# Optimization experiments

Measured on AMD Instinct MI355X. Metric: run time of the kernel, lower is better.

The kernel has to match this reference:

```python
import jax, jax.numpy as jnp
import numpy as np

NUM_HEADS = 32
MICRO_BATCHES = 2
TOP_K = 2
LN_EPS = 1e-5


def _mha(x, scale, bias, wq, wk, wv, wo):
    # Pre-LN multi-head self-attention with residual (RealSelfAttention).
    B, S, D = x.shape
    H = NUM_HEADS
    hd = D // H
    res = x
    mu = jnp.mean(x, axis=-1, keepdims=True)
    xc = x - mu
    var = jnp.mean(xc * xc, axis=-1, keepdims=True)
    xn = xc / jnp.sqrt(var + LN_EPS) * scale + bias
    q = (xn @ wq.T).reshape(B, S, H, hd).transpose(0, 2, 1, 3)
    k = (xn @ wk.T).reshape(B, S, H, hd).transpose(0, 2, 1, 3)
    v = (xn @ wv.T).reshape(B, S, H, hd).transpose(0, 2, 1, 3)
    scores = jnp.einsum('bhqd,bhkd->bhqk', q, k) * (1.0 / np.sqrt(hd).astype(np.float32))
    attn = jax.nn.softmax(scores, axis=-1)
    o = jnp.einsum('bhqk,bhkd->bhqd', attn, v).transpose(0, 2, 1, 3).reshape(B, S, D)
    return o @ wo.T + res


def setup_inputs() -> dict:
    key = jax.random.key(0)
    D, E, F = 1024, 8, 4096
    B, S = 4, 1024
    ks = jax.random.split(key, 16)
    w = lambda k, shape: (jax.random.normal(k, shape, dtype=jnp.float32) * 0.02)
    return {
        'x': jax.random.normal(ks[0], (B, S, D), dtype=jnp.float32),
        'ln1_scale': jnp.ones((D,), jnp.float32),
        'ln1_bias': jnp.zeros((D,), jnp.float32),
        'wq1': w(ks[1], (D, D)), 'wk1': w(ks[2], (D, D)),
        'wv1': w(ks[3], (D, D)), 'wo1': w(ks[4], (D, D)),
        'gate_w': w(ks[5], (E, D)),
        'exp_w1': w(ks[6], (E, F, D)), 'exp_b1': jnp.zeros((E, F), jnp.float32),
        'exp_w2': w(ks[7], (E, D, F)), 'exp_b2': jnp.zeros((E, D), jnp.float32),
        'ln2_scale': jnp.ones((D,), jnp.float32),
        'ln2_bias': jnp.zeros((D,), jnp.float32),
        'wq2': w(ks[8], (D, D)), 'wk2': w(ks[9], (D, D)),
        'wv2': w(ks[10], (D, D)), 'wo2': w(ks[11], (D, D)),
    }


def reference(x, ln1_scale, ln1_bias, wq1, wk1, wv1, wo1, gate_w,
              exp_w1, exp_b1, exp_w2, exp_b2,
              ln2_scale, ln2_bias, wq2, wk2, wv2, wo2):
    B, S, D = x.shape
    E = exp_w1.shape[0]
    # PreOps: attention layer L (per-sample, so full-batch apply == per-microbatch apply)
    y = _mha(x, ln1_scale, ln1_bias, wq1, wk1, wv1, wo1)
    # Gate: logits + top-k indices computed in source but never applied to tokens.
    flat = y.reshape(B * S, D)
    logits = flat @ gate_w.T
    _ = jax.lax.top_k(logits, TOP_K)  # indices unused downstream (faithful to source)
    # Dispatch (all_to_all on 1 device == identity): per-microbatch flat tokens are
    # chunked equally across local experts.
    T = (B // MICRO_BATCHES) * S            # tokens per microbatch
    toks = y.reshape(MICRO_BATCHES, E, T // E, D)
    h = jax.nn.gelu(jnp.einsum('metd,efd->metf', toks, exp_w1) + exp_b1[None, :, None, :],
                    approximate=False)
    eo = jnp.einsum('metf,edf->metd', h, exp_w2) + exp_b2[None, :, None, :]
    # Combine (identity) + PostOps: attention layer L+1
    z = eo.reshape(B, S, D)
    out = _mha(z, ln2_scale, ln2_bias, wq2, wk2, wv2, wo2)
    return out
```

## Files before the change

### kernel.cpp

```cpp
#include <hip/hip_runtime.h>

typedef __attribute__((ext_vector_type(8))) short bf16x8;
typedef __attribute__((ext_vector_type(4))) float f32x4;
typedef __attribute__((ext_vector_type(4))) short short4v;

#define DEV __device__ __forceinline__

DEV short f2bf(float f) {
  union { float f; unsigned u; } x; x.f = f;
  unsigned r = x.u + 0x7fffu + ((x.u >> 16) & 1u);
  return (short)(r >> 16);
}

#define GL2LDS16(g, l) __builtin_amdgcn_global_load_lds(                      \
    (const __attribute__((address_space(1))) void*)(g),                       \
    (__attribute__((address_space(3))) void*)(l), 16, 0, 0)

__global__ __launch_bounds__(256) void k_cast_bf16(const float* __restrict__ s,
                                                   short* __restrict__ d, int n4) {
  int i = blockIdx.x * 256 + threadIdx.x;
  if (i >= n4) return;
  float4 v = ((const float4*)s)[i];
  short4v o;
  o[0] = f2bf(v.x); o[1] = f2bf(v.y); o[2] = f2bf(v.z); o[3] = f2bf(v.w);
  ((short4v*)d)[i] = o;
}

__global__ __launch_bounds__(256)
void k_ln(const float* __restrict__ X, const float* __restrict__ G,
          const float* __restrict__ Bi, short* __restrict__ Y) {
  const int row = blockIdx.x, t = threadIdx.x;
  const float4 v = ((const float4*)(X + (size_t)row * 1024))[t];
  float s = v.x + v.y + v.z + v.w;
  float s2 = v.x * v.x + v.y * v.y + v.z * v.z + v.w * v.w;
#pragma unroll
  for (int m = 1; m < 64; m <<= 1) { s += __shfl_xor(s, m); s2 += __shfl_xor(s2, m); }
  __shared__ float rs[4], rq[4];
  const int w = t >> 6, lane = t & 63;
  if (lane == 0) { rs[w] = s; rq[w] = s2; }
  __syncthreads();
  s = rs[0] + rs[1] + rs[2] + rs[3];
  s2 = rq[0] + rq[1] + rq[2] + rq[3];
  const float mu = s * (1.f / 1024.f);
  const float var = s2 * (1.f / 1024.f) - mu * mu;
  const float rstd = rsqrtf(var + 1e-5f);
  const float4 g = ((const float4*)G)[t];
  const float4 bi = ((const float4*)Bi)[t];
  short4v o;
  o[0] = f2bf((v.x - mu) * rstd * g.x + bi.x);
  o[1] = f2bf((v.y - mu) * rstd * g.y + bi.y);
  o[2] = f2bf((v.z - mu) * rstd * g.z + bi.z);
  o[3] = f2bf((v.w - mu) * rstd * g.w + bi.w);
  ((short4v*)(Y + (size_t)row * 1024))[t] = o;
}

template <int EPI, int EXPERT, int BN>
__global__ __launch_bounds__(256)
void k_gemm_bt(const short* __restrict__ A, const short* __restrict__ Bt,
               void* __restrict__ Cv, const float* __restrict__ Res,
               const float* __restrict__ Bias, int M, int N, int K) {
  constexpr int NF = BN / 32;
  constexpr int BR = BN / 64;
  __shared__ __attribute__((aligned(16))) short As[2][128 * 32];
  __shared__ __attribute__((aligned(16))) short Bs[2][BN * 32];
  const int tid = threadIdx.x;
  const int w = tid >> 6, lane = tid & 63;
  const int r16 = lane & 15, kg = lane >> 4;
  const int wr = w >> 1, wc = w & 1;

  size_t rowBase = (size_t)blockIdx.y * 128;
  size_t bOff = 0, biasOff = 0;
  if constexpr (EXPERT) {
    int e = blockIdx.z >> 1, mb = blockIdx.z & 1;
    rowBase += (size_t)(mb * 8 + e) * 256;
    bOff = (size_t)e * N * K;
    biasOff = (size_t)e * N;
  }
  const size_t col0 = (size_t)blockIdx.x * BN;
  const short* Ab = A + rowBase * K;
  const short* Bb = Bt + bOff + col0 * K;

  f32x4 acc[4][NF] = {};

  auto stage = [&](int buf, int k0) {
#pragma unroll
    for (int i = 0; i < 2; ++i) {
      int c = (i * 4 + w) * 64 + lane;
      int row = c >> 2;
      int sl = (c & 3) ^ (row & 3);
      GL2LDS16(Ab + (size_t)row * K + k0 + sl * 8, (char*)As[buf] + (size_t)(i * 4 + w) * 1024);
    }
#pragma unroll
    for (int i = 0; i < BR; ++i) {
      int c = (i * 4 + w) * 64 + lane;
      int row = c >> 2;
      int sl = (c & 3) ^ (row & 3);
      GL2LDS16(Bb + (size_t)row * K + k0 + sl * 8, (char*)Bs[buf] + (size_t)(i * 4 + w) * 1024);
    }
  };

  stage(0, 0);
  __syncthreads();
  int cur = 0;
  for (int k0 = 0; k0 < K; k0 += 32) {
    if (k0 + 32 < K) stage(cur ^ 1, k0 + 32);
    bf16x8 af[4], bg[NF];
#pragma unroll
    for (int m = 0; m < 4; ++m) {
      int row = wr * 64 + m * 16 + r16;
      af[m] = *(const bf16x8*)(As[cur] + row * 32 + (kg ^ (row & 3)) * 8);
    }
#pragma unroll
    for (int n = 0; n < NF; ++n) {
      int row = wc * (BN / 2) + n * 16 + r16;
      bg[n] = *(const bf16x8*)(Bs[cur] + row * 32 + (kg ^ (row & 3)) * 8);
    }
#pragma unroll
    for (int m = 0; m < 4; ++m)
#pragma unroll
      for (int n = 0; n < NF; ++n)
        acc[m][n] = __builtin_amdgcn_mfma_f32_16x16x32_bf16(af[m], bg[n], acc[m][n], 0, 0, 0);
    __syncthreads();
    cur ^= 1;
  }

#pragma unroll
  for (int m = 0; m < 4; ++m) {
    size_t grow0 = rowBase + wr * 64 + m * 16 + kg * 4;
#pragma unroll
    for (int n = 0; n < NF; ++n) {
      size_t gcol = col0 + wc * (BN / 2) + n * 16 + r16;
#pragma unroll
      for (int r = 0; r < 4; ++r) {
        size_t idx = (grow0 + r) * (size_t)N + gcol;
        float v = acc[m][n][r];
        if constexpr (EPI == 1 || EPI == 4) v += Res[idx];
        if constexpr (EPI == 2 || EPI == 3) v += Bias[biasOff + gcol];
        if constexpr (EPI == 2) v = 0.5f * v * (1.f + erff(v * 0.70710678118654752f));
        if constexpr (EPI <= 2) ((short*)Cv)[idx] = f2bf(v);
        else                    ((float*)Cv)[idx] = v;
      }
    }
  }
}

__global__ __launch_bounds__(256, 3)
void k_attn(const short* __restrict__ QKV, short* __restrict__ O) {
  const int qt = blockIdx.x, h = blockIdx.y, b = blockIdx.z;
  const int tid = threadIdx.x, w = tid >> 6, lane = tid & 63;
  const int r16 = lane & 15, kg = lane >> 4;

  __shared__ __attribute__((aligned(16))) short Kl[2][128 * 32];
  __shared__ __attribute__((aligned(16))) short Vt[2][32 * 128];
  __shared__ __attribute__((aligned(16))) short Pl[4][16 * 128];

  const size_t tb = (size_t)b * 1024;
  const int qbase = qt * 128 + w * 32;

  bf16x8 aq[2];
#pragma unroll
  for (int f = 0; f < 2; ++f)
    aq[f] = *(const bf16x8*)(QKV + (tb + qbase + f * 16 + r16) * 3072 + h * 32 + kg * 8);

  f32x4 acc[2][2] = {};
  float lreg[2][4] = {};
  const float scale = 0.17677669529663687f;

  auto stageK = [&](int bid, int kc) {
#pragma unroll
    for (int i = 0; i < 2; ++i) {
      int c = (i * 4 + w) * 64 + lane;
      int row = c >> 2;
      int sl = (c & 3) ^ (row & 3);
      GL2LDS16(QKV + (tb + kc * 128 + row) * 3072 + 1024 + h * 32 + sl * 8,
               (char*)Kl[bid] + (size_t)(i * 4 + w) * 1024);
    }
  };

  stageK(0, 0);
  {
    int c0 = tid,        vr0 = c0 >> 2, d00 = (c0 & 3) * 8;
    int c1 = 256 + tid,  vr1 = c1 >> 2, d01 = (c1 & 3) * 8;
    bf16x8 v0 = *(const bf16x8*)(QKV + (tb + vr0) * 3072 + 2048 + h * 32 + d00);
    bf16x8 v1 = *(const bf16x8*)(QKV + (tb + vr1) * 3072 + 2048 + h * 32 + d01);
#pragma unroll
    for (int j = 0; j < 8; ++j) {
      int da = d00 + j, db = d01 + j;
      Vt[0][((da * 128 + vr0) ^ ((da & 7) << 3))] = v0[j];
      Vt[0][((db * 128 + vr1) ^ ((db & 7) << 3))] = v1[j];
    }
  }
  __syncthreads();

  int bi = 0;
  for (int kc = 0; kc < 8; ++kc) {
    bf16x8 nv0, nv1;
    int nvr0 = 0, nd0 = 0, nvr1 = 0, nd1 = 0;
    if (kc < 7) {
      stageK(bi ^ 1, kc + 1);
      const short* Vg = QKV + (tb + (size_t)(kc + 1) * 128) * 3072 + 2048 + h * 32;
      int c0 = tid;       nvr0 = c0 >> 2; nd0 = (c0 & 3) * 8;
      int c1 = 256 + tid; nvr1 = c1 >> 2; nd1 = (c1 & 3) * 8;
      nv0 = *(const bf16x8*)(Vg + (size_t)nvr0 * 3072 + nd0);
      nv1 = *(const bf16x8*)(Vg + (size_t)nvr1 * 3072 + nd1);
    }

    f32x4 s[2][8];
#pragma unroll
    for (int kt = 0; kt < 8; ++kt) {
      int row = kt * 16 + r16;
      bf16x8 bk = *(const bf16x8*)(Kl[bi] + row * 32 + (kg ^ (row & 3)) * 8);
      f32x4 zz = {0.f, 0.f, 0.f, 0.f};
      s[0][kt] = __builtin_amdgcn_mfma_f32_16x16x32_bf16(aq[0], bk, zz, 0, 0, 0);
      s[1][kt] = __builtin_amdgcn_mfma_f32_16x16x32_bf16(aq[1], bk, zz, 0, 0, 0);
    }

#pragma unroll
    for (int f = 0; f < 2; ++f)
#pragma unroll
      for (int r = 0; r < 4; ++r) {
        float sum = 0.f;
#pragma unroll
        for (int kt = 0; kt < 8; ++kt) {
          float p = __expf(s[f][kt][r] * scale);
          s[f][kt][r] = p;
          sum += p;
        }
#pragma unroll
        for (int m = 1; m < 16; m <<= 1) sum += __shfl_xor(sum, m);
        lreg[f][r] += sum;
      }

    short* P = Pl[w];
#pragma unroll
    for (int f = 0; f < 2; ++f) {
#pragma unroll
      for (int kt = 0; kt < 8; ++kt)
#pragma unroll
        for (int r = 0; r < 4; ++r) {
          int row = kg * 4 + r;
          P[((row * 128 + kt * 16 + r16) ^ ((row & 7) << 3))] = f2bf(s[f][kt][r]);
        }
#pragma unroll
      for (int ks = 0; ks < 4; ++ks) {
        bf16x8 pa = *(const bf16x8*)(P + ((r16 * 128 + ks * 32 + kg * 8) ^ ((r16 & 7) << 3)));
#pragma unroll
        for (int dt = 0; dt < 2; ++dt) {
          int vrow = dt * 16 + r16;
          bf16x8 bv = *(const bf16x8*)(Vt[bi] + ((vrow * 128 + ks * 32 + kg * 8) ^ ((vrow & 7) << 3)));
          acc[f][dt] = __builtin_amdgcn_mfma_f32_16x16x32_bf16(pa, bv, acc[f][dt], 0, 0, 0);
        }
      }
    }

    if (kc < 7) {
#pragma unroll
      for (int j = 0; j < 8; ++j) {
        int da = nd0 + j, db = nd1 + j;
        Vt[bi ^ 1][((da * 128 + nvr0) ^ ((da & 7) << 3))] = nv0[j];
        Vt[bi ^ 1][((db * 128 + nvr1) ^ ((db & 7) << 3))] = nv1[j];
      }
    }

    __syncthreads();
    bi ^= 1;
  }

#pragma unroll
  for (int f = 0; f < 2; ++f)
#pragma unroll
    for (int r = 0; r < 4; ++r) {
      float inv = 1.f / lreg[f][r];
      size_t qrow = tb + qbase + f * 16 + kg * 4 + r;
#pragma unroll
      for (int dt = 0; dt < 2; ++dt)
        O[qrow * 1024 + h * 32 + dt * 16 + r16] = f2bf(acc[f][dt][r] * inv);
    }
}

extern "C" void kernel_launch(void* const* d_in, const int* in_sizes, int n_in,
                              void* d_out, int out_size, void* d_ws, size_t ws_size,
                              hipStream_t stream) {
  const float* x    = (const float*)d_in[0];
  const float* ln1s = (const float*)d_in[1];
  const float* ln1b = (const float*)d_in[2];
  const float* wq1  = (const float*)d_in[3];
  const float* wk1  = (const float*)d_in[4];
  const float* wv1  = (const float*)d_in[5];
  const float* wo1  = (const float*)d_in[6];
  const float* ew1  = (const float*)d_in[8];
  const float* eb1  = (const float*)d_in[9];
  const float* ew2  = (const float*)d_in[10];
  const float* eb2  = (const float*)d_in[11];
  const float* ln2s = (const float*)d_in[12];
  const float* ln2b = (const float*)d_in[13];
  const float* wq2  = (const float*)d_in[14];
  const float* wk2  = (const float*)d_in[15];
  const float* wv2  = (const float*)d_in[16];
  const float* wo2  = (const float*)d_in[17];

  char* ws = (char*)d_ws;
  size_t off = 0;
  auto alloc = [&](size_t bytes) {
    char* p = ws + off;
    off += (bytes + 255) & ~(size_t)255;
    return p;
  };
  short* wqkv1b = (short*)alloc(3072ull * 1024 * 2);
  short* wo1b   = (short*)alloc(1024ull * 1024 * 2);
  short* wqkv2b = (short*)alloc(3072ull * 1024 * 2);
  short* wo2b   = (short*)alloc(1024ull * 1024 * 2);
  short* ew1b   = (short*)alloc(8ull * 4096 * 1024 * 2);
  short* ew2b   = (short*)alloc(8ull * 1024 * 4096 * 2);
  short* xnb    = (short*)alloc(4096ull * 1024 * 2);
  short* qkvo   = (short*)alloc(4096ull * 4096 * 2);
  short* ybf    = (short*)alloc(4096ull * 1024 * 2);
  float* zf     = (float*)alloc(4096ull * 1024 * 4);
  (void)ws_size; (void)in_sizes; (void)n_in; (void)out_size;

  short* QKV = qkvo;
  short* Ob  = qkvo + 4096ull * 3072;
  short* hb  = qkvo;

  auto cast = [&](const float* s, short* d, size_t n) {
    int n4 = (int)(n / 4);
    k_cast_bf16<<<(n4 + 255) / 256, 256, 0, stream>>>(s, d, n4);
  };
  cast(wq1, wqkv1b,           1048576);
  cast(wk1, wqkv1b + 1048576, 1048576);
  cast(wv1, wqkv1b + 2097152, 1048576);
  cast(wo1, wo1b,             1048576);
  cast(wq2, wqkv2b,           1048576);
  cast(wk2, wqkv2b + 1048576, 1048576);
  cast(wv2, wqkv2b + 2097152, 1048576);
  cast(wo2, wo2b,             1048576);
  cast(ew1, ew1b, 8ull * 4096 * 1024);
  cast(ew2, ew2b, 8ull * 1024 * 4096);

  k_ln<<<4096, 256, 0, stream>>>(x, ln1s, ln1b, xnb);
  k_gemm_bt<0, 0, 128><<<dim3(24, 32, 1), 256, 0, stream>>>(xnb, wqkv1b, QKV, nullptr, nullptr, 4096, 3072, 1024);
  k_attn<<<dim3(8, 32, 4), 256, 0, stream>>>(QKV, Ob);
  k_gemm_bt<1, 0, 64><<<dim3(16, 32, 1), 256, 0, stream>>>(Ob, wo1b, ybf, x, nullptr, 4096, 1024, 1024);
  k_gemm_bt<2, 1, 128><<<dim3(32, 2, 16), 256, 0, stream>>>(ybf, ew1b, hb, nullptr, eb1, 256, 4096, 1024);
  k_gemm_bt<3, 1, 64><<<dim3(16, 2, 16), 256, 0, stream>>>(hb, ew2b, zf, nullptr, eb2, 256, 1024, 4096);
  k_ln<<<4096, 256, 0, stream>>>(zf, ln2s, ln2b, xnb);
  k_gemm_bt<0, 0, 128><<<dim3(24, 32, 1), 256, 0, stream>>>(xnb, wqkv2b, QKV, nullptr, nullptr, 4096, 3072, 1024);
  k_attn<<<dim3(8, 32, 4), 256, 0, stream>>>(QKV, Ob);
  k_gemm_bt<4, 0, 64><<<dim3(16, 32, 1), 256, 0, stream>>>(Ob, wo2b, (float*)d_out, zf, nullptr, 4096, 1024, 1024);
}
```

Before: 574.8 us.

## Fuse fp32 expert-weight conversion into GEMM loads and remap block indices

Removes the separate cast kernels for the two large expert weight tensors (64M floats). The expert GEMMs now read fp32 weights directly into registers, convert them to bf16 and write them to LDS after the MFMA step, so the load overlaps compute. All grids become 1D with a remapped block order, which groups blocks sharing weight tiles (expert-interleaved, and row tiles grouped by 8 for the dense GEMMs) to improve L2 reuse. The expert GEMMs now read twice the weight bytes per tile through register-staged loads instead of async global-to-LDS, which raises register pressure.

Result: faster. 543.1 us (-5.5%).

```diff
diff --git a/kernel.cpp b/kernel.cpp
--- a/kernel.cpp
+++ b/kernel.cpp
@@ -54,11 +54,11 @@
   ((short4v*)(Y + (size_t)row * 1024))[t] = o;
 }
 
-template <int EPI, int EXPERT, int BN>
+template <int EPI, int EXPERT, int BN, int BF32>
 __global__ __launch_bounds__(256)
-void k_gemm_bt(const short* __restrict__ A, const short* __restrict__ Bt,
+void k_gemm_bt(const short* __restrict__ A, const void* __restrict__ Btv,
                void* __restrict__ Cv, const float* __restrict__ Res,
-               const float* __restrict__ Bias, int M, int N, int K) {
+               const float* __restrict__ Bias, int M, int N, int K, int xt) {
   constexpr int NF = BN / 32;
   constexpr int BR = BN / 64;
   __shared__ __attribute__((aligned(16))) short As[2][128 * 32];
@@ -68,21 +68,29 @@
   const int r16 = lane & 15, kg = lane >> 4;
   const int wr = w >> 1, wc = w & 1;
 
-  size_t rowBase = (size_t)blockIdx.y * 128;
-  size_t bOff = 0, biasOff = 0;
+  const int bid = blockIdx.x;
+  int bx;
+  size_t rowBase, bOff = 0, biasOff = 0;
   if constexpr (EXPERT) {
-    int e = blockIdx.z >> 1, mb = blockIdx.z & 1;
-    rowBase += (size_t)(mb * 8 + e) * 256;
+    int e = bid & 7, mb = (bid >> 3) & 1, by = (bid >> 4) & 1;
+    bx = bid >> 5;
+    rowBase = (size_t)by * 128 + (size_t)(mb * 8 + e) * 256;
     bOff = (size_t)e * N * K;
     biasOff = (size_t)e * N;
-  }
-  const size_t col0 = (size_t)blockIdx.x * BN;
+  } else {
+    int y7 = bid & 7, r = bid >> 3;
+    bx = r % xt;
+    rowBase = (size_t)(y7 + 8 * (r / xt)) * 128;
+  }
+  const size_t col0 = (size_t)bx * BN;
   const short* Ab = A + rowBase * K;
-  const short* Bb = Bt + bOff + col0 * K;
+  const short* Bb16 = (const short*)Btv + bOff + col0 * K;
+  const float* Bb32 = (const float*)Btv + bOff + col0 * K;
 
   f32x4 acc[4][NF] = {};
-
-  auto stage = [&](int buf, int k0) {
+  float4 nb[BR][2];
+
+  auto stageA = [&](int buf, int k0) {
 #pragma unroll
     for (int i = 0; i < 2; ++i) {
       int c = (i * 4 + w) * 64 + lane;
@@ -90,20 +98,49 @@
       int sl = (c & 3) ^ (row & 3);
       GL2LDS16(Ab + (size_t)row * K + k0 + sl * 8, (char*)As[buf] + (size_t)(i * 4 + w) * 1024);
     }
+  };
+  auto stageB16 = [&](int buf, int k0) {
 #pragma unroll
     for (int i = 0; i < BR; ++i) {
       int c = (i * 4 + w) * 64 + lane;
       int row = c >> 2;
       int sl = (c & 3) ^ (row & 3);
-      GL2LDS16(Bb + (size_t)row * K + k0 + sl * 8, (char*)Bs[buf] + (size_t)(i * 4 + w) * 1024);
-    }
-  };
-
-  stage(0, 0);
+      GL2LDS16(Bb16 + (size_t)row * K + k0 + sl * 8, (char*)Bs[buf] + (size_t)(i * 4 + w) * 1024);
+    }
+  };
+  auto loadB32 = [&](int k0) {
+#pragma unroll
+    for (int i = 0; i < BR; ++i) {
+      int c = (i * 4 + w) * 64 + lane;
+      int row = c >> 2;
+      int sl = (c & 3) ^ (row & 3);
+      const float* src = Bb32 + (size_t)row * K + k0 + sl * 8;
+      nb[i][0] = *(const float4*)src;
+      nb[i][1] = *(const float4*)(src + 4);
+    }
+  };
+  auto writeB32 = [&](int buf) {
+#pragma unroll
+    for (int i = 0; i < BR; ++i) {
+      union { short s[8]; bf16x8 v; } o;
+      o.s[0] = f2bf(nb[i][0].x); o.s[1] = f2bf(nb[i][0].y);
+      o.s[2] = f2bf(nb[i][0].z); o.s[3] = f2bf(nb[i][0].w);
+      o.s[4] = f2bf(nb[i][1].x); o.s[5] = f2bf(nb[i][1].y);
+      o.s[6] = f2bf(nb[i][1].z); o.s[7] = f2bf(nb[i][1].w);
+      *(bf16x8*)((char*)Bs[buf] + (size_t)(i * 4 + w) * 1024 + (size_t)lane * 16) = o.v;
+    }
+  };
+
+  stageA(0, 0);
+  if constexpr (BF32) { loadB32(0); writeB32(0); } else { stageB16(0, 0); }
   __syncthreads();
   int cur = 0;
   for (int k0 = 0; k0 < K; k0 += 32) {
-    if (k0 + 32 < K) stage(cur ^ 1, k0 + 32);
+    const bool nxt = (k0 + 32 < K);
+    if (nxt) {
+      stageA(cur ^ 1, k0 + 32);
+      if constexpr (BF32) loadB32(k0 + 32); else stageB16(cur ^ 1, k0 + 32);
+    }
     bf16x8 af[4], bg[NF];
 #pragma unroll
     for (int m = 0; m < 4; ++m) {
@@ -120,6 +157,7 @@
 #pragma unroll
       for (int n = 0; n < NF; ++n)
         acc[m][n] = __builtin_amdgcn_mfma_f32_16x16x32_bf16(af[m], bg[n], acc[m][n], 0, 0, 0);
+    if (nxt) { if constexpr (BF32) writeB32(cur ^ 1); }
     __syncthreads();
     cur ^= 1;
   }
@@ -142,11 +180,13 @@
       }
     }
   }
+  (void)M;
 }
 
 __global__ __launch_bounds__(256, 3)
 void k_attn(const short* __restrict__ QKV, short* __restrict__ O) {
-  const int qt = blockIdx.x, h = blockIdx.y, b = blockIdx.z;
+  const int bid = blockIdx.x;
+  const int qt = bid >> 7, h = bid & 31, b = (bid >> 5) & 3;
   const int tid = threadIdx.x, w = tid >> 6, lane = tid & 63;
   const int r16 = lane & 15, kg = lane >> 4;
 
@@ -166,14 +206,14 @@
   float lreg[2][4] = {};
   const float scale = 0.17677669529663687f;
 
-  auto stageK = [&](int bid, int kc) {
+  auto stageK = [&](int bid2, int kc) {
 #pragma unroll
     for (int i = 0; i < 2; ++i) {
       int c = (i * 4 + w) * 64 + lane;
       int row = c >> 2;
       int sl = (c & 3) ^ (row & 3);
       GL2LDS16(QKV + (tb + kc * 128 + row) * 3072 + 1024 + h * 32 + sl * 8,
-               (char*)Kl[bid] + (size_t)(i * 4 + w) * 1024);
+               (char*)Kl[bid2] + (size_t)(i * 4 + w) * 1024);
     }
   };
 
@@ -310,8 +350,6 @@
   short* wo1b   = (short*)alloc(1024ull * 1024 * 2);
   short* wqkv2b = (short*)alloc(3072ull * 1024 * 2);
   short* wo2b   = (short*)alloc(1024ull * 1024 * 2);
-  short* ew1b   = (short*)alloc(8ull * 4096 * 1024 * 2);
-  short* ew2b   = (short*)alloc(8ull * 1024 * 4096 * 2);
   short* xnb    = (short*)alloc(4096ull * 1024 * 2);
   short* qkvo   = (short*)alloc(4096ull * 4096 * 2);
   short* ybf    = (short*)alloc(4096ull * 1024 * 2);
@@ -334,17 +372,15 @@
   cast(wk2, wqkv2b + 1048576, 1048576);
   cast(wv2, wqkv2b + 2097152, 1048576);
   cast(wo2, wo2b,             1048576);
-  cast(ew1, ew1b, 8ull * 4096 * 1024);
-  cast(ew2, ew2b, 8ull * 1024 * 4096);
 
   k_ln<<<4096, 256, 0, stream>>>(x, ln1s, ln1b, xnb);
-  k_gemm_bt<0, 0, 128><<<dim3(24, 32, 1), 256, 0, stream>>>(xnb, wqkv1b, QKV, nullptr, nullptr, 4096, 3072, 1024);
-  k_attn<<<dim3(8, 32, 4), 256, 0, stream>>>(QKV, Ob);
-  k_gemm_bt<1, 0, 64><<<dim3(16, 32, 1), 256, 0, stream>>>(Ob, wo1b, ybf, x, nullptr, 4096, 1024, 1024);
-  k_gemm_bt<2, 1, 128><<<dim3(32, 2, 16), 256, 0, stream>>>(ybf, ew1b, hb, nullptr, eb1, 256, 4096, 1024);
-  k_gemm_bt<3, 1, 64><<<dim3(16, 2, 16), 256, 0, stream>>>(hb, ew2b, zf, nullptr, eb2, 256, 1024, 4096);
+  k_gemm_bt<0, 0, 128, 0><<<768, 256, 0, stream>>>(xnb, wqkv1b, QKV, nullptr, nullptr, 4096, 3072, 1024, 24);
+  k_attn<<<1024, 256, 0, stream>>>(QKV, Ob);
+  k_gemm_bt<1, 0, 64, 0><<<512, 256, 0, stream>>>(Ob, wo1b, ybf, x, nullptr, 4096, 1024, 1024, 16);
+  k_gemm_bt<2, 1, 128, 1><<<1024, 256, 0, stream>>>(ybf, ew1, hb, nullptr, eb1, 256, 4096, 1024, 0);
+  k_gemm_bt<3, 1, 64, 1><<<512, 256, 0, stream>>>(hb, ew2, zf, nullptr, eb2, 256, 1024, 4096, 0);
   k_ln<<<4096, 256, 0, stream>>>(zf, ln2s, ln2b, xnb);
-  k_gemm_bt<0, 0, 128><<<dim3(24, 32, 1), 256, 0, stream>>>(xnb, wqkv2b, QKV, nullptr, nullptr, 4096, 3072, 1024);
-  k_attn<<<dim3(8, 32, 4), 256, 0, stream>>>(QKV, Ob);
-  k_gemm_bt<4, 0, 64><<<dim3(16, 32, 1), 256, 0, stream>>>(Ob, wo2b, (float*)d_out, zf, nullptr, 4096, 1024, 1024);
-}
+  k_gemm_bt<0, 0, 128, 0><<<768, 256, 0, stream>>>(xnb, wqkv2b, QKV, nullptr, nullptr, 4096, 3072, 1024, 24);
+  k_attn<<<1024, 256, 0, stream>>>(QKV, Ob);
+  k_gemm_bt<4, 0, 64, 0><<<512, 256, 0, stream>>>(Ob, wo2b, (float*)d_out, zf, nullptr, 4096, 1024, 1024, 16);
+}
```
